# Performance work log

Measured on AMD Instinct MI355X. Metric: run time of the kernel, lower is better.

The kernel has to match this reference:

```python
import jax, jax.numpy as jnp
import numpy as np

B, T, C, H = 8, 2048, 768, 12
D = C // H

def setup_inputs() -> dict:
    key = jax.random.key(0)
    ks = jax.random.split(key, 5)
    s = 0.02
    return {
        "x": jax.random.normal(ks[0], (B, T, C), dtype=jnp.float32),
        "w_attn": jax.random.normal(ks[1], (C, 3 * C), dtype=jnp.float32) * s,
        "b_attn": jnp.zeros((3 * C,), dtype=jnp.float32),
        "w_proj": jax.random.normal(ks[2], (C, C), dtype=jnp.float32) * s,
        "b_proj": jnp.zeros((C,), dtype=jnp.float32),
    }

def reference(x, w_attn, b_attn, w_proj, b_proj):
    Bx, Tx, Cx = x.shape
    qkv = x @ w_attn + b_attn                       # [B,T,3C]
    q, k, v = jnp.split(qkv, 3, axis=-1)
    # [B,H,T,D]
    q = q.reshape(Bx, Tx, H, D).transpose(0, 2, 1, 3)
    k = k.reshape(Bx, Tx, H, D).transpose(0, 2, 1, 3)
    v = v.reshape(Bx, Tx, H, D).transpose(0, 2, 1, 3)
    scale = 1.0 / jnp.sqrt(jnp.float32(D))
    att = jnp.einsum('bhqd,bhkd->bhqk', q, k) * scale
    causal = jnp.tril(jnp.ones((Tx, Tx), dtype=bool))
    att = jnp.where(causal[None, None], att, -jnp.inf)
    att = jax.nn.softmax(att, axis=-1)
    y = jnp.einsum('bhqk,bhkd->bhqd', att, v)
    y = y.transpose(0, 2, 1, 3).reshape(Bx, Tx, Cx)
    y = y @ w_proj + b_proj
    return y, k, v
```

## Files before the change

### kernel.cpp

```cpp
#include <hip/hip_runtime.h>
#include <hip/hip_bf16.h>
#include <stdint.h>

#define Bz 8
#define Tz 2048
#define Cz 768
#define Hz 12
#define Dz 64
#define Mz (Bz*Tz)
#define N3 (3*Cz)
#define YSZ ((size_t)Mz*Cz)

#define SCL 0.18033688011112042f
#define KVB 64
#define QBLK 256

typedef __bf16 bf16;
typedef __attribute__((ext_vector_type(8))) bf16 bf16x8;
typedef __attribute__((ext_vector_type(4))) bf16 bf16x4;
typedef __attribute__((ext_vector_type(4))) float f32x4;

#define MFMA(A_,B_,C_) __builtin_amdgcn_mfma_f32_16x16x32_bf16(A_,B_,C_,0,0,0)

__device__ __forceinline__ void gll16(const void* g, void* l) {
  __builtin_amdgcn_global_load_lds(
      (const __attribute__((address_space(1))) void*)g,
      (__attribute__((address_space(3))) void*)l, 16, 0, 0);
}

__global__ __launch_bounds__(256) void prep_x(const float* __restrict__ x,
                                              bf16* __restrict__ xb) {
  int i = blockIdx.x*blockDim.x + threadIdx.x;
  int stride = gridDim.x*blockDim.x;
  const float4* x4 = (const float4*)x;
  int n4 = (int)(YSZ/4);
  for (int j = i; j < n4; j += stride) {
    float4 f = x4[j];
    bf16x4 o = { (bf16)f.x, (bf16)f.y, (bf16)f.z, (bf16)f.w };
    *(bf16x4*)(xb + 4*(size_t)j) = o;
  }
}

__global__ __launch_bounds__(256) void transpose_conv(const float* __restrict__ src,
                                                      bf16* __restrict__ dst,
                                                      int R, int Ncol) {
  __shared__ float tile[32][33];
  int bx = blockIdx.x, by = blockIdx.y;
  int tx = threadIdx.x & 31, ty = threadIdx.x >> 5;
  #pragma unroll
  for (int i = 0; i < 4; ++i)
    tile[ty + 8*i][tx] = src[(size_t)(by*32 + ty + 8*i)*Ncol + bx*32 + tx];
  __syncthreads();
  #pragma unroll
  for (int i = 0; i < 4; ++i)
    dst[(size_t)(bx*32 + ty + 8*i)*R + by*32 + tx] = (bf16)tile[tx][ty + 8*i];
}

template<int EPI>
__global__ __launch_bounds__(256) void gemm128(
    const bf16* __restrict__ A, const bf16* __restrict__ Bt,
    int Kdim, int Mtiles, int Ntiles,
    const float* __restrict__ bias,
    bf16* __restrict__ qws, bf16* __restrict__ kws, bf16* __restrict__ vtb,
    float* __restrict__ kout, float* __restrict__ vout,
    float* __restrict__ yout)
{
  __shared__ alignas(16) bf16 sA[2][128*64];
  __shared__ alignas(16) bf16 sB[2][128*64];
  int nwg = Mtiles*Ntiles;
  int bid = blockIdx.x;
  int cpx = nwg >> 3;
  int swz = (bid & 7)*cpx + (bid >> 3);
  int ntile = swz % Ntiles, mtile = swz / Ntiles;
  int tid = threadIdx.x, w = tid >> 6, l = tid & 63;
  int wr = w >> 1, wc = w & 1;
  const int rowBase = mtile*128, colBase = ntile*128;

  f32x4 acc[4][4] = {};

  int rbase = tid >> 3;
  int ch    = tid & 7;
  int swk   = (ch ^ (rbase & 7)) << 3;
  const bf16* gA = A + (size_t)(rowBase + rbase)*Kdim + swk;
  const bf16* gB = Bt + (size_t)(colBase + rbase)*Kdim + swk;

  int lr = l & 15, lg = l >> 4;
  int nK = Kdim >> 6;

  {
    char* lA = (char*)sA[0] + w*1024;
    char* lB = (char*)sB[0] + w*1024;
    #pragma unroll
    for (int p = 0; p < 4; ++p) {
      gll16(gA + (size_t)(p*32)*Kdim, lA + p*4096);
      gll16(gB + (size_t)(p*32)*Kdim, lB + p*4096);
    }
    gA += 64; gB += 64;
  }
  int buf = 0;
  for (int t = 0; t < nK; ++t) {
    if (t + 1 < nK) {
      char* lA = (char*)sA[buf ^ 1] + w*1024;
      char* lB = (char*)sB[buf ^ 1] + w*1024;
      #pragma unroll
      for (int p = 0; p < 4; ++p) {
        gll16(gA + (size_t)(p*32)*Kdim, lA + p*4096);
        gll16(gB + (size_t)(p*32)*Kdim, lB + p*4096);
      }
      gA += 64; gB += 64;
      asm volatile("s_waitcnt vmcnt(8)" ::: "memory");
    } else {
      asm volatile("s_waitcnt vmcnt(0)" ::: "memory");
    }
    __builtin_amdgcn_s_barrier();
    __builtin_amdgcn_sched_barrier(0);
    const char* cA = (const char*)sA[buf];
    const char* cB = (const char*)sB[buf];
    __builtin_amdgcn_s_setprio(1);
    #pragma unroll
    for (int kk = 0; kk < 2; ++kk) {
      bf16x8 af[4], bfr[4];
      int cc = ((kk*4 + lg) ^ (lr & 7)) << 4;
      #pragma unroll
      for (int m = 0; m < 4; ++m)
        af[m] = *(const bf16x8*)(cA + (wr*64 + m*16 + lr)*128 + cc);
      #pragma unroll
      for (int n = 0; n < 4; ++n)
        bfr[n] = *(const bf16x8*)(cB + (wc*64 + n*16 + lr)*128 + cc);
      #pragma unroll
      for (int m = 0; m < 4; ++m)
        #pragma unroll
        for (int n = 0; n < 4; ++n)
          acc[m][n] = MFMA(af[m], bfr[n], acc[m][n]);
    }
    __builtin_amdgcn_s_setprio(0);
    asm volatile("s_waitcnt lgkmcnt(0)" ::: "memory");
    __builtin_amdgcn_s_barrier();
    __builtin_amdgcn_sched_barrier(0);
    buf ^= 1;
  }

  #pragma unroll
  for (int m = 0; m < 4; ++m) {
    #pragma unroll
    for (int n = 0; n < 4; ++n) {
      int gcol = colBase + wc*64 + n*16 + lr;
      float bv = bias[gcol];
      int grow0 = rowBase + wr*64 + m*16 + lg*4;
      if (EPI == 1) {
        #pragma unroll
        for (int r = 0; r < 4; ++r)
          yout[(size_t)(grow0 + r)*Cz + gcol] = acc[m][n][r] + bv;
      } else {
        int which = gcol / Cz;
        int within = gcol - which*Cz;
        int h = within >> 6, d = within & 63;
        int bidx = grow0 >> 11;
        int t0 = grow0 & 2047;
        size_t bhTD = ((size_t)bidx*Hz + h);
        if (which == 0) {
          bf16* qp = qws + (bhTD*Tz + t0)*Dz + d;
          #pragma unroll
          for (int r = 0; r < 4; ++r)
            qp[(size_t)r*Dz] = (bf16)((acc[m][n][r] + bv) * SCL);
        } else if (which == 1) {
          float* kp = kout + (bhTD*Tz + t0)*Dz + d;
          bf16*  kp2 = kws + (bhTD*Tz + t0)*Dz + d;
          #pragma unroll
          for (int r = 0; r < 4; ++r) {
            float v = acc[m][n][r] + bv;
            kp[(size_t)r*Dz] = v;
            kp2[(size_t)r*Dz] = (bf16)v;
          }
        } else {
          float* vp = vout + (bhTD*Tz + t0)*Dz + d;
          bf16x4 pk;
          #pragma unroll
          for (int r = 0; r < 4; ++r) {
            float v = acc[m][n][r] + bv;
            vp[(size_t)r*Dz] = v;
            pk[r] = (bf16)v;
          }
          int ts = (t0 & ~31) | (((t0 >> 2) & 3) << 3) | (((t0 >> 4) & 1) << 2) | (t0 & 3);
          *(bf16x4*)(vtb + (bhTD*Dz + d)*Tz + ts) = pk;
        }
      }
    }
  }
}

__device__ __forceinline__ void attn_tile(
    int kv0, int qminw, int qmaxw, int q_l, int lr, int lg,
    const char* cK, const char* cV,
    const bf16x8& qf0, const bf16x8& qf1, const bf16x8& ones,
    f32x4 (&o)[4], f32x4& lsum)
{
  const f32x4 zf = {0.f, 0.f, 0.f, 0.f};
  f32x4 s[4];
  __builtin_amdgcn_s_setprio(1);
  #pragma unroll
  for (int n = 0; n < 4; ++n) {
    int kvb = kv0 + n*16;
    if (kvb <= qmaxw) {
      int row = n*16 + lr;
      int c0 = lg ^ (lr & 7);
      bf16x8 kf0 = *(const bf16x8*)(cK + row*128 + (c0 << 4));
      bf16x8 kf1 = *(const bf16x8*)(cK + row*128 + ((c0 ^ 4) << 4));
      f32x4 t = MFMA(kf0, qf0, zf);
      s[n] = MFMA(kf1, qf1, t);
    } else {
      s[n][0] = -1e30f; s[n][1] = -1e30f; s[n][2] = -1e30f; s[n][3] = -1e30f;
    }
  }
  __builtin_amdgcn_s_setprio(0);
  #pragma unroll
  for (int n = 0; n < 4; ++n) {
    int kvb = kv0 + n*16;
    if (kvb <= qmaxw && kvb + 15 > qminw) {
      #pragma unroll
      for (int r = 0; r < 4; ++r)
        s[n][r] = (kvb + 4*lg + r <= q_l) ? s[n][r] : -1e30f;
    }
  }
  #pragma unroll
  for (int n = 0; n < 4; ++n) {
    #pragma unroll
    for (int r = 0; r < 4; ++r)
      s[n][r] = exp2f(s[n][r]);
  }
  __builtin_amdgcn_s_setprio(1);
  #pragma unroll
  for (int kk = 0; kk < 2; ++kk) {
    if (kv0 + kk*32 <= qmaxw) {
      bf16x8 pf;
      pf[0] = (bf16)s[2*kk][0];   pf[1] = (bf16)s[2*kk][1];
      pf[2] = (bf16)s[2*kk][2];   pf[3] = (bf16)s[2*kk][3];
      pf[4] = (bf16)s[2*kk+1][0]; pf[5] = (bf16)s[2*kk+1][1];
      pf[6] = (bf16)s[2*kk+1][2]; pf[7] = (bf16)s[2*kk+1][3];
      lsum = MFMA(pf, ones, lsum);
      int cb = (kk*4 + lg) ^ (lr & 7);
      #pragma unroll
      for (int nd = 0; nd < 4; ++nd) {
        bf16x8 vf = *(const bf16x8*)(cV + (nd*16 + lr)*128 + (cb << 4));
        o[nd] = MFMA(pf, vf, o[nd]);
      }
    }
  }
  __builtin_amdgcn_s_setprio(0);
}

__global__ __launch_bounds__(1024, 4) void attn128(
    const bf16* __restrict__ qws, const bf16* __restrict__ kb,
    const bf16* __restrict__ vtb, bf16* __restrict__ yatt)
{
  __shared__ alignas(16) char sK[2][8192];
  __shared__ alignas(16) char sV[2][8192];
  int bid = blockIdx.x;
  int qb = (Tz/QBLK) - 1 - bid/(Bz*Hz);
  int bh = bid % (Bz*Hz);
  int b = bh / Hz, h = bh - b*Hz;
  int tid = threadIdx.x, w = tid >> 6, l = tid & 63;
  int lr = l & 15, lg = l >> 4;
  const int q0 = qb*QBLK;
  const int qminw = q0 + w*16;
  const int qmaxw = qminw + 15;
  const int q_l = qminw + lr;

  const bf16* qbase = qws + ((size_t)bh*Tz + qminw + lr)*Dz + lg*8;
  bf16x8 qf0 = *(const bf16x8*)qbase;
  bf16x8 qf1 = *(const bf16x8*)(qbase + 32);

  bf16 onev = (bf16)1.0f;
  bf16x8 ones = { onev, onev, onev, onev, onev, onev, onev, onev };

  f32x4 o[4] = {};
  f32x4 lsum = {0.f, 0.f, 0.f, 0.f};

  bool isK = tid < 512;
  int soff = (tid & 511) * 16;
  int srow = soff >> 7;
  int sch  = (soff >> 4) & 7;
  int ssw  = ((sch ^ (srow & 7)) << 3);
  const bf16* sp = isK ? (kb  + (size_t)bh*Tz*Dz + (size_t)srow*Dz + ssw)
                       : (vtb + (size_t)bh*Dz*Tz + (size_t)srow*Tz + ssw);
  ptrdiff_t sstride = isK ? (ptrdiff_t)KVB*Dz : (ptrdiff_t)KVB;
  char* d0 = isK ? (sK[0] + w*1024) : (sV[0] + (w - 8)*1024);
  char* d1 = isK ? (sK[1] + w*1024) : (sV[1] + (w - 8)*1024);

  int nT = 4*qb + 4;
  gll16(sp, d0); sp += sstride;

  int buf = 0;
  for (int kt = 0; kt < nT; ++kt) {
    if (kt + 1 < nT) {
      gll16(sp, buf ? d0 : d1); sp += sstride;
      asm volatile("s_waitcnt vmcnt(1)" ::: "memory");
    } else {
      asm volatile("s_waitcnt vmcnt(0)" ::: "memory");
    }
    __builtin_amdgcn_s_barrier();
    __builtin_amdgcn_sched_barrier(0);
    attn_tile(kt*KVB, qminw, qmaxw, q_l, lr, lg, sK[buf], sV[buf],
              qf0, qf1, ones, o, lsum);
    if (kt + 1 < nT) {
      asm volatile("s_waitcnt lgkmcnt(0)" ::: "memory");
      __builtin_amdgcn_s_barrier();
      __builtin_amdgcn_sched_barrier(0);
    }
    buf ^= 1;
  }

  f32x4 inv;
  #pragma unroll
  for (int r = 0; r < 4; ++r) inv[r] = 1.0f / lsum[r];
  #pragma unroll
  for (int nd = 0; nd < 4; ++nd) {
    int d = nd*16 + lr;
    int t0 = q0 + w*16 + lg*4;
    bf16* yp = yatt + ((size_t)(b*Tz + t0))*Cz + h*Dz + d;
    yp[0*Cz]   = (bf16)(o[nd][0] * inv[0]);
    yp[1*Cz]   = (bf16)(o[nd][1] * inv[1]);
    yp[2*Cz]   = (bf16)(o[nd][2] * inv[2]);
    yp[3*Cz]   = (bf16)(o[nd][3] * inv[3]);
  }
}

extern "C" void kernel_launch(void* const* d_in, const int* in_sizes, int n_in,
                              void* d_out, int out_size, void* d_ws, size_t ws_size,
                              hipStream_t stream) {
  const float* x      = (const float*)d_in[0];
  const float* w_attn = (const float*)d_in[1];
  const float* b_attn = (const float*)d_in[2];
  const float* w_proj = (const float*)d_in[3];
  const float* b_proj = (const float*)d_in[4];

  float* y    = (float*)d_out;
  float* kout = y + YSZ;
  float* vout = y + 2*YSZ;

  char* ws = (char*)d_ws;
  bf16* xb   = (bf16*)ws;
  bf16* qws  = (bf16*)(ws + 25165824);
  bf16* kb   = (bf16*)(ws + 50331648);
  bf16* vtb  = (bf16*)(ws + 75497472);
  bf16* wtA  = (bf16*)(ws + 100663296);
  bf16* wtP  = (bf16*)(ws + 104202240);
  bf16* yatt = xb;

  prep_x<<<2048, 256, 0, stream>>>(x, xb);
  transpose_conv<<<dim3(N3/32, Cz/32), 256, 0, stream>>>(w_attn, wtA, Cz, N3);
  transpose_conv<<<dim3(Cz/32, Cz/32), 256, 0, stream>>>(w_proj, wtP, Cz, Cz);

  gemm128<0><<<dim3((Mz/128)*(N3/128)), 256, 0, stream>>>(
      xb, wtA, Cz, Mz/128, N3/128, b_attn, qws, kb, vtb, kout, vout, nullptr);

  attn128<<<dim3((Tz/QBLK)*(Bz*Hz)), 1024, 0, stream>>>(qws, kb, vtb, yatt);

  gemm128<1><<<dim3((Mz/128)*(Cz/128)), 256, 0, stream>>>(
      yatt, wtP, Cz, Mz/128, Cz/128, b_proj, nullptr, nullptr, nullptr,
      nullptr, nullptr, y);
}
```

Baseline: 258.9 us.

## Enlarge GEMM tiles to 256x256 with 8 waves and trim masked attention work

Both projection GEMMs move from 128x128 tiles with 4 waves to 256x256 tiles with 8 waves. Each wave now computes 128x64 outputs, which raises arithmetic intensity per shared-memory load, and the A fragments are loaded in two halves with a waitcnt before the MFMAs. The attention tile helper now returns early when a KV block lies fully beyond the causal limit, and it skips exp2 on fully masked sub-blocks by writing zeros. The trade-off is more LDS (128KB) and more registers per block, fewer workgroups (the projection GEMM gets only 192 blocks), and a possible drop in occupancy.

```diff
diff --git a/kernel.cpp b/kernel.cpp
--- a/kernel.cpp
+++ b/kernel.cpp
@@ -57,7 +57,7 @@
 }
 
 template<int EPI>
-__global__ __launch_bounds__(256) void gemm128(
+__global__ __launch_bounds__(512, 2) void gemm256(
     const bf16* __restrict__ A, const bf16* __restrict__ Bt,
     int Kdim, int Mtiles, int Ntiles,
     const float* __restrict__ bias,
@@ -65,18 +65,18 @@
     float* __restrict__ kout, float* __restrict__ vout,
     float* __restrict__ yout)
 {
-  __shared__ alignas(16) bf16 sA[2][128*64];
-  __shared__ alignas(16) bf16 sB[2][128*64];
+  __shared__ alignas(16) bf16 sA[2][256*64];
+  __shared__ alignas(16) bf16 sB[2][256*64];
   int nwg = Mtiles*Ntiles;
   int bid = blockIdx.x;
   int cpx = nwg >> 3;
   int swz = (bid & 7)*cpx + (bid >> 3);
   int ntile = swz % Ntiles, mtile = swz / Ntiles;
   int tid = threadIdx.x, w = tid >> 6, l = tid & 63;
-  int wr = w >> 1, wc = w & 1;
-  const int rowBase = mtile*128, colBase = ntile*128;
-
-  f32x4 acc[4][4] = {};
+  int wr = w >> 2, wc = w & 3;
+  const int rowBase = mtile*256, colBase = ntile*256;
+
+  f32x4 acc[8][4] = {};
 
   int rbase = tid >> 3;
   int ch    = tid & 7;
@@ -92,8 +92,8 @@
     char* lB = (char*)sB[0] + w*1024;
     #pragma unroll
     for (int p = 0; p < 4; ++p) {
-      gll16(gA + (size_t)(p*32)*Kdim, lA + p*4096);
-      gll16(gB + (size_t)(p*32)*Kdim, lB + p*4096);
+      gll16(gA + (size_t)(p*64)*Kdim, lA + p*8192);
+      gll16(gB + (size_t)(p*64)*Kdim, lB + p*8192);
     }
     gA += 64; gB += 64;
   }
@@ -104,8 +104,8 @@
       char* lB = (char*)sB[buf ^ 1] + w*1024;
       #pragma unroll
       for (int p = 0; p < 4; ++p) {
-        gll16(gA + (size_t)(p*32)*Kdim, lA + p*4096);
-        gll16(gB + (size_t)(p*32)*Kdim, lB + p*4096);
+        gll16(gA + (size_t)(p*64)*Kdim, lA + p*8192);
+        gll16(gB + (size_t)(p*64)*Kdim, lB + p*8192);
       }
       gA += 64; gB += 64;
       asm volatile("s_waitcnt vmcnt(8)" ::: "memory");
@@ -116,37 +116,45 @@
     __builtin_amdgcn_sched_barrier(0);
     const char* cA = (const char*)sA[buf];
     const char* cB = (const char*)sB[buf];
-    __builtin_amdgcn_s_setprio(1);
     #pragma unroll
     for (int kk = 0; kk < 2; ++kk) {
-      bf16x8 af[4], bfr[4];
-      int cc = ((kk*4 + lg) ^ (lr & 7)) << 4;
-      #pragma unroll
-      for (int m = 0; m < 4; ++m)
-        af[m] = *(const bf16x8*)(cA + (wr*64 + m*16 + lr)*128 + cc);
-      #pragma unroll
-      for (int n = 0; n < 4; ++n)
-        bfr[n] = *(const bf16x8*)(cB + (wc*64 + n*16 + lr)*128 + cc);
-      #pragma unroll
-      for (int m = 0; m < 4; ++m)
+      bf16x8 bfr[4];
+      #pragma unroll
+      for (int n = 0; n < 4; ++n) {
+        int row = wc*64 + n*16 + lr;
+        bfr[n] = *(const bf16x8*)(cB + row*128 + (((kk*4 + lg) ^ (row & 7)) << 4));
+      }
+      #pragma unroll
+      for (int mh = 0; mh < 2; ++mh) {
+        bf16x8 af[4];
         #pragma unroll
-        for (int n = 0; n < 4; ++n)
-          acc[m][n] = MFMA(af[m], bfr[n], acc[m][n]);
-    }
-    __builtin_amdgcn_s_setprio(0);
-    asm volatile("s_waitcnt lgkmcnt(0)" ::: "memory");
+        for (int mm = 0; mm < 4; ++mm) {
+          int row = wr*128 + (mh*4 + mm)*16 + lr;
+          af[mm] = *(const bf16x8*)(cA + row*128 + (((kk*4 + lg) ^ (row & 7)) << 4));
+        }
+        asm volatile("s_waitcnt lgkmcnt(0)" ::: "memory");
+        __builtin_amdgcn_sched_barrier(0);
+        __builtin_amdgcn_s_setprio(1);
+        #pragma unroll
+        for (int mm = 0; mm < 4; ++mm)
+          #pragma unroll
+          for (int n = 0; n < 4; ++n)
+            acc[mh*4 + mm][n] = MFMA(af[mm], bfr[n], acc[mh*4 + mm][n]);
+        __builtin_amdgcn_s_setprio(0);
+      }
+    }
     __builtin_amdgcn_s_barrier();
     __builtin_amdgcn_sched_barrier(0);
     buf ^= 1;
   }
 
   #pragma unroll
-  for (int m = 0; m < 4; ++m) {
+  for (int m = 0; m < 8; ++m) {
     #pragma unroll
     for (int n = 0; n < 4; ++n) {
       int gcol = colBase + wc*64 + n*16 + lr;
       float bv = bias[gcol];
-      int grow0 = rowBase + wr*64 + m*16 + lg*4;
+      int grow0 = rowBase + wr*128 + m*16 + lg*4;
       if (EPI == 1) {
         #pragma unroll
         for (int r = 0; r < 4; ++r)
@@ -195,6 +203,7 @@
     const bf16x8& qf0, const bf16x8& qf1, const bf16x8& ones,
     f32x4 (&o)[4], f32x4& lsum)
 {
+  if (kv0 > qmaxw) return;
   const f32x4 zf = {0.f, 0.f, 0.f, 0.f};
   f32x4 s[4];
   __builtin_amdgcn_s_setprio(1);
@@ -208,25 +217,26 @@
       bf16x8 kf1 = *(const bf16x8*)(cK + row*128 + ((c0 ^ 4) << 4));
       f32x4 t = MFMA(kf0, qf0, zf);
       s[n] = MFMA(kf1, qf1, t);
-    } else {
-      s[n][0] = -1e30f; s[n][1] = -1e30f; s[n][2] = -1e30f; s[n][3] = -1e30f;
     }
   }
   __builtin_amdgcn_s_setprio(0);
   #pragma unroll
   for (int n = 0; n < 4; ++n) {
     int kvb = kv0 + n*16;
-    if (kvb <= qmaxw && kvb + 15 > qminw) {
+    if (kvb <= qmaxw) {
+      if (kvb + 15 > qminw) {
+        #pragma unroll
+        for (int r = 0; r < 4; ++r)
+          s[n][r] = (kvb + 4*lg + r <= q_l) ? s[n][r] : -1e30f;
+      }
       #pragma unroll
       for (int r = 0; r < 4; ++r)
-        s[n][r] = (kvb + 4*lg + r <= q_l) ? s[n][r] : -1e30f;
-    }
-  }
-  #pragma unroll
-  for (int n = 0; n < 4; ++n) {
-    #pragma unroll
-    for (int r = 0; r < 4; ++r)
-      s[n][r] = exp2f(s[n][r]);
+        s[n][r] = exp2f(s[n][r]);
+    } else {
+      #pragma unroll
+      for (int r = 0; r < 4; ++r)
+        s[n][r] = 0.f;
+    }
   }
   __builtin_amdgcn_s_setprio(1);
   #pragma unroll
@@ -351,12 +361,12 @@
   transpose_conv<<<dim3(N3/32, Cz/32), 256, 0, stream>>>(w_attn, wtA, Cz, N3);
   transpose_conv<<<dim3(Cz/32, Cz/32), 256, 0, stream>>>(w_proj, wtP, Cz, Cz);
 
-  gemm128<0><<<dim3((Mz/128)*(N3/128)), 256, 0, stream>>>(
-      xb, wtA, Cz, Mz/128, N3/128, b_attn, qws, kb, vtb, kout, vout, nullptr);
+  gemm256<0><<<dim3((Mz/256)*(N3/256)), 512, 0, stream>>>(
+      xb, wtA, Cz, Mz/256, N3/256, b_attn, qws, kb, vtb, kout, vout, nullptr);
 
   attn128<<<dim3((Tz/QBLK)*(Bz*Hz)), 1024, 0, stream>>>(qws, kb, vtb, yatt);
 
-  gemm128<1><<<dim3((Mz/128)*(Cz/128)), 256, 0, stream>>>(
-      yatt, wtP, Cz, Mz/128, Cz/128, b_proj, nullptr, nullptr, nullptr,
+  gemm256<1><<<dim3((Mz/256)*(Cz/256)), 512, 0, stream>>>(
+      yatt, wtP, Cz, Mz/256, Cz/256, b_proj, nullptr, nullptr, nullptr,
       nullptr, nullptr, y);
 }
```

Result: slower. 282.0 us (+8.9%).
